# Kernel optimization log

Measured on AMD Instinct MI355X. Metric: run time of the kernel, lower is better.

## Reference

```python
import jax, jax.numpy as jnp
import numpy as np
from math import sqrt

B, S, D, H = 2, 2048, 1024, 16
HD = D // H


def setup_inputs() -> dict:
    key = jax.random.key(0)
    ks = jax.random.split(key, 5)
    std = 0.02
    return {
        "tensor_in": jax.random.normal(ks[0], (B, S, D), dtype=jnp.float32),
        "attention_mask": jnp.zeros((1, 1, S, S), dtype=jnp.float32),
        "Wq": jax.random.normal(ks[1], (D, D), dtype=jnp.float32) * std,
        "Wk": jax.random.normal(ks[2], (D, D), dtype=jnp.float32) * std,
        "Wv": jax.random.normal(ks[3], (D, D), dtype=jnp.float32) * std,
        "Wo": jax.random.normal(ks[4], (D, D), dtype=jnp.float32) * std,
    }


def reference(tensor_in, attention_mask, Wq, Wk, Wv, Wo):
    # nn.Linear(dim, dim, bias=False): y = x @ W.T, W is [out, in]
    q = tensor_in @ Wq.T  # [B,S,D]
    k = tensor_in @ Wk.T
    v = tensor_in @ Wv.T
    # split heads -> [B,H,S,HD]
    q = q.reshape(B, S, H, HD).transpose(0, 2, 1, 3)
    k = k.reshape(B, S, H, HD).transpose(0, 2, 1, 3)
    v = v.reshape(B, S, H, HD).transpose(0, 2, 1, 3)
    # scores [B,H,S,S]; note: mask added BEFORE scaling, scale = sqrt(full dim)
    scores = jnp.einsum("bhqd,bhkd->bhqk", q, k) + attention_mask
    weights = jax.nn.softmax(scores / sqrt(D), axis=-1)  # dropout = identity (eval)
    context = jnp.einsum("bhqk,bhkd->bhqd", weights, v)
    context = context.transpose(0, 2, 1, 3).reshape(B, S, D)
    return context @ Wo.T
```

## Files before the change

kernel.cpp:

```cpp
#include <hip/hip_runtime.h>

#define B_  2
#define S_  2048
#define D_  1024
#define H_  16
#define HD_ 64
#define M_  (B_*S_)

typedef __attribute__((ext_vector_type(8))) short  short8;
typedef __attribute__((ext_vector_type(4))) float  float4v;
typedef __attribute__((ext_vector_type(4))) int    int4v;
typedef __attribute__((ext_vector_type(4))) unsigned short ushort4v;

#define PSCALE 0.0450843341f

__device__ __forceinline__ unsigned short f_to_bf16bits(float f) {
    unsigned int x = __builtin_bit_cast(unsigned int, f);
    unsigned int lsb = (x >> 16) & 1u;
    x += 0x7fffu + lsb;
    return (unsigned short)(x >> 16);
}

__device__ __forceinline__ float fast_exp2(float x) {
#if __has_builtin(__builtin_amdgcn_exp2f)
    return __builtin_amdgcn_exp2f(x);
#else
    return exp2f(x);
#endif
}

__global__ __launch_bounds__(256) void cvt_bf16(
    const float* __restrict__ X,  const float* __restrict__ Wq,
    const float* __restrict__ Wk, const float* __restrict__ Wv,
    const float* __restrict__ Wo,
    unsigned short* __restrict__ Xb,  unsigned short* __restrict__ Wqb,
    unsigned short* __restrict__ Wkb, unsigned short* __restrict__ Wvb,
    unsigned short* __restrict__ Wob)
{
    const long t = (long)blockIdx.x * 256 + threadIdx.x;
    const long e = t * 8;
    const float* src; unsigned short* dst; long off;
    if      (e < 4194304) { src = X;  dst = Xb;  off = e; }
    else if (e < 5242880) { src = Wq; dst = Wqb; off = e - 4194304; }
    else if (e < 6291456) { src = Wk; dst = Wkb; off = e - 5242880; }
    else if (e < 7340032) { src = Wv; dst = Wvb; off = e - 6291456; }
    else                  { src = Wo; dst = Wob; off = e - 7340032; }
    float4v a = *(const float4v*)&src[off];
    float4v b = *(const float4v*)&src[off + 4];
    int4v o;
    o[0] = (int)f_to_bf16bits(a[0]) | ((int)f_to_bf16bits(a[1]) << 16);
    o[1] = (int)f_to_bf16bits(a[2]) | ((int)f_to_bf16bits(a[3]) << 16);
    o[2] = (int)f_to_bf16bits(b[0]) | ((int)f_to_bf16bits(b[1]) << 16);
    o[3] = (int)f_to_bf16bits(b[2]) | ((int)f_to_bf16bits(b[3]) << 16);
    *(int4v*)&dst[off] = o;
}

__global__ __launch_bounds__(256) void gemm_bt(
    const unsigned short* __restrict__ A,
    const unsigned short* __restrict__ B0,
    const unsigned short* __restrict__ B1,
    const unsigned short* __restrict__ B2,
    void* __restrict__ O0, void* __restrict__ O1, void* __restrict__ O2,
    int mode_base)
{
    const int K = 1024;
    const int z = blockIdx.z;
    const int mode = mode_base + z;
    const unsigned short* Aop;
    const unsigned short* Bop;
    void* Op = (z == 0) ? O0 : (z == 1) ? O1 : O2;
    int m0, n0;
    if (mode == 2) {
        Aop = B2; Bop = A;
        m0 = blockIdx.y * 128;
        n0 = blockIdx.x * 128;
    } else {
        Aop = A;
        Bop = (z == 0) ? B0 : (z == 1) ? B1 : B2;
        m0 = blockIdx.x * 128;
        n0 = blockIdx.y * 128;
    }

    __shared__ alignas(16) unsigned short As[128 * 64];
    __shared__ alignas(16) unsigned short Bs[128 * 64];

    const int tid  = threadIdx.x;
    const int wv   = tid >> 6;
    const int lane = tid & 63;
    const int wm   = wv >> 1, wn = wv & 1;
    const int q4   = lane >> 4, l15 = lane & 15;

    const unsigned short* gA[4];
    const unsigned short* gB[4];
    int ldsoff[4];
#pragma unroll
    for (int j = 0; j < 4; j++) {
        const int r = wv * 32 + j * 8 + (lane >> 3);
        const int c = (((lane & 7) ^ (r & 7)) * 8);
        gA[j] = Aop + (long)(m0 + r) * K + c;
        gB[j] = Bop + (long)(n0 + r) * K + c;
        ldsoff[j] = (wv * 32 + j * 8) * 64 + lane * 8;
    }

    int aoff[2][4], boff[2][4];
#pragma unroll
    for (int ks = 0; ks < 2; ks++)
#pragma unroll
        for (int t = 0; t < 4; t++) {
            const int swz = (((ks * 4 + q4) ^ (l15 & 7)) * 8);
            aoff[ks][t] = (wm * 64 + t * 16 + l15) * 64 + swz;
            boff[ks][t] = (wn * 64 + t * 16 + l15) * 64 + swz;
        }

    float4v acc[4][4];
#pragma unroll
    for (int i = 0; i < 4; i++)
#pragma unroll
        for (int j = 0; j < 4; j++) acc[i][j] = (float4v)0.0f;

    int4v ar[4], br[4];
#pragma unroll
    for (int j = 0; j < 4; j++) {
        ar[j] = *(const int4v*)gA[j];
        br[j] = *(const int4v*)gB[j];
        gA[j] += 64; gB[j] += 64;
    }

    for (int k0 = 0; k0 < K; k0 += 64) {
        __syncthreads();
#pragma unroll
        for (int j = 0; j < 4; j++) {
            *(int4v*)&As[ldsoff[j]] = ar[j];
            *(int4v*)&Bs[ldsoff[j]] = br[j];
        }
        __syncthreads();

        if (k0 + 64 < K) {
#pragma unroll
            for (int j = 0; j < 4; j++) {
                ar[j] = *(const int4v*)gA[j];
                br[j] = *(const int4v*)gB[j];
                gA[j] += 64; gB[j] += 64;
            }
        }

#pragma unroll
        for (int ks = 0; ks < 2; ks++) {
            short8 afr[4], bfr[4];
#pragma unroll
            for (int mt = 0; mt < 4; mt++) afr[mt] = *(const short8*)&As[aoff[ks][mt]];
#pragma unroll
            for (int nt = 0; nt < 4; nt++) bfr[nt] = *(const short8*)&Bs[boff[ks][nt]];
#pragma unroll
            for (int mt = 0; mt < 4; mt++)
#pragma unroll
                for (int nt = 0; nt < 4; nt++)
                    acc[mt][nt] = __builtin_amdgcn_mfma_f32_16x16x32_bf16(
                        afr[mt], bfr[nt], acc[mt][nt], 0, 0, 0);
        }
    }

#pragma unroll
    for (int mt = 0; mt < 4; mt++)
#pragma unroll
        for (int nt = 0; nt < 4; nt++)
#pragma unroll
            for (int r = 0; r < 4; r++) {
                const int m = m0 + wm * 64 + mt * 16 + q4 * 4 + r;
                const int n = n0 + wn * 64 + nt * 16 + l15;
                float v = acc[mt][nt][r];
                if (mode == 3) {
                    ((float*)Op)[(long)m * D_ + n] = v;
                } else if (mode == 2) {
                    const long off = (((long)(n >> 11) * H_ + (m >> 6)) * HD_ + (m & 63)) * S_ + (n & 2047);
                    ((unsigned short*)Op)[off] = f_to_bf16bits(v);
                } else {
                    const long off = ((long)((m >> 11) * H_ + (n >> 6)) * S_ + (m & 2047)) * HD_ + (n & 63);
                    if (mode == 0) v *= PSCALE;
                    ((unsigned short*)Op)[off] = f_to_bf16bits(v);
                }
            }
}

__global__ __launch_bounds__(256) void attn(
    const unsigned short* __restrict__ Q,
    const unsigned short* __restrict__ Kk,
    const unsigned short* __restrict__ Vt,
    const float* __restrict__ mask,
    unsigned short* __restrict__ ctx)
{
    __shared__ alignas(16) unsigned short Ks[64 * 64];
    __shared__ alignas(16) unsigned short Vs[64 * 64];
    __shared__ alignas(16) unsigned short Ps[4][16 * 64];

    const int tid  = threadIdx.x;
    const int wv   = tid >> 6;
    const int lane = tid & 63;
    const int q4   = lane >> 4, l15 = lane & 15;
    const int bh   = blockIdx.x;
    const int q0   = blockIdx.y * 64;

    const long head = (long)bh * S_ * HD_;

    const int qrow = q0 + wv * 16 + l15;
    short8 qfr[2];
    qfr[0] = *(const short8*)&Q[head + (long)qrow * HD_ + q4 * 8];
    qfr[1] = *(const short8*)&Q[head + (long)qrow * HD_ + 32 + q4 * 8];

    float l_acc[4];
#pragma unroll
    for (int r = 0; r < 4; r++) l_acc[r] = 0.0f;
    float4v oacc[4];
#pragma unroll
    for (int dt = 0; dt < 4; dt++) oacc[dt] = (float4v)0.0f;

    const int row0 = tid >> 3, row1 = row0 + 32, sch = tid & 7;
    const int cc   = ((sch ^ (row0 & 7)) * 8);
    const unsigned short* gK0 = Kk + head + (long)row0 * HD_ + cc;
    const unsigned short* gK1 = Kk + head + (long)row1 * HD_ + cc;
    const unsigned short* gV0 = Vt + head + (long)row0 * S_  + cc;
    const unsigned short* gV1 = Vt + head + (long)row1 * S_  + cc;
    const int ldsOff0 = row0 * 64 + sch * 8;
    const int ldsOff1 = row1 * 64 + sch * 8;

    const float* mrow[4];
#pragma unroll
    for (int r = 0; r < 4; r++)
        mrow[r] = mask + (long)(q0 + wv * 16 + q4 * 4 + r) * S_ + l15;

    float mv[4][4];
#pragma unroll
    for (int nt = 0; nt < 4; nt++)
#pragma unroll
        for (int r = 0; r < 4; r++) mv[nt][r] = mrow[r][nt * 16];

    const int pswz = (q4 & 1) * 4;
    const int psl3 = l15 >> 3;

    for (int k0 = 0; k0 < S_; k0 += 64) {
        __syncthreads();
        *(int4v*)&Ks[ldsOff0] = *(const int4v*)(gK0 + (long)k0 * HD_);
        *(int4v*)&Ks[ldsOff1] = *(const int4v*)(gK1 + (long)k0 * HD_);
        *(int4v*)&Vs[ldsOff0] = *(const int4v*)(gV0 + k0);
        *(int4v*)&Vs[ldsOff1] = *(const int4v*)(gV1 + k0);
        __syncthreads();

        float4v sfr[4];
#pragma unroll
        for (int nt = 0; nt < 4; nt++) {
            const int row = nt * 16 + l15;
            const int p0 = ((q4       ^ (row & 7)) * 8);
            const int p1 = (((4 + q4) ^ (row & 7)) * 8);
            short8 kb0 = *(const short8*)&Ks[row * 64 + p0];
            short8 kb1 = *(const short8*)&Ks[row * 64 + p1];
            float4v s = (float4v)0.0f;
            s = __builtin_amdgcn_mfma_f32_16x16x32_bf16(qfr[0], kb0, s, 0, 0, 0);
            s = __builtin_amdgcn_mfma_f32_16x16x32_bf16(qfr[1], kb1, s, 0, 0, 0);
            sfr[nt] = s;
        }

        float mvn[4][4];
        const int knext = (k0 + 64 < S_) ? k0 + 64 : k0;
#pragma unroll
        for (int nt = 0; nt < 4; nt++)
#pragma unroll
            for (int r = 0; r < 4; r++) mvn[nt][r] = mrow[r][knext + nt * 16];

#pragma unroll
        for (int nt = 0; nt < 4; nt++)
#pragma unroll
            for (int r = 0; r < 4; r++) {
                const float p = fast_exp2(fmaf(mv[nt][r], PSCALE, sfr[nt][r]));
                l_acc[r] += p;
                const int c8 = (nt * 2 + psl3) ^ (pswz + r);
                Ps[wv][(q4 * 4 + r) * 64 + c8 * 8 + (l15 & 7)] = f_to_bf16bits(p);
            }

        const int pp0 = ((q4       ^ (l15 & 7)) * 8);
        const int pp1 = (((4 + q4) ^ (l15 & 7)) * 8);
        short8 pf0 = *(const short8*)&Ps[wv][l15 * 64 + pp0];
        short8 pf1 = *(const short8*)&Ps[wv][l15 * 64 + pp1];

#pragma unroll
        for (int dt = 0; dt < 4; dt++) {
            const int row = dt * 16 + l15;
            const int p0 = ((q4       ^ (row & 7)) * 8);
            const int p1 = (((4 + q4) ^ (row & 7)) * 8);
            short8 vb0 = *(const short8*)&Vs[row * 64 + p0];
            short8 vb1 = *(const short8*)&Vs[row * 64 + p1];
            float4v o = oacc[dt];
            o = __builtin_amdgcn_mfma_f32_16x16x32_bf16(pf0, vb0, o, 0, 0, 0);
            o = __builtin_amdgcn_mfma_f32_16x16x32_bf16(pf1, vb1, o, 0, 0, 0);
            oacc[dt] = o;
        }

#pragma unroll
        for (int nt = 0; nt < 4; nt++)
#pragma unroll
            for (int r = 0; r < 4; r++) mv[nt][r] = mvn[nt][r];
    }

#pragma unroll
    for (int r = 0; r < 4; r++) {
#pragma unroll
        for (int off = 1; off < 16; off <<= 1)
            l_acc[r] += __shfl_xor(l_acc[r], off);
    }

    const int b = bh >> 4, h = bh & 15;
#pragma unroll
    for (int dt = 0; dt < 4; dt++)
#pragma unroll
        for (int r = 0; r < 4; r++) {
            const int qg = q0 + wv * 16 + q4 * 4 + r;
            const int d  = dt * 16 + l15;
            const float v = oacc[dt][r] / l_acc[r];
            ctx[((long)(b * S_ + qg)) * D_ + h * HD_ + d] = f_to_bf16bits(v);
        }
}

extern "C" void kernel_launch(void* const* d_in, const int* in_sizes, int n_in,
                              void* d_out, int out_size, void* d_ws, size_t ws_size,
                              hipStream_t stream) {
    const float* X    = (const float*)d_in[0];
    const float* mask = (const float*)d_in[1];
    const float* Wq   = (const float*)d_in[2];
    const float* Wk   = (const float*)d_in[3];
    const float* Wv   = (const float*)d_in[4];
    const float* Wo   = (const float*)d_in[5];
    float* out        = (float*)d_out;

    unsigned short* ws = (unsigned short*)d_ws;
    unsigned short* qws  = ws;
    unsigned short* kws  = ws + 4194304;
    unsigned short* vtws = ws + 8388608;
    unsigned short* ctx  = ws + 12582912;
    unsigned short* Xb   = ws + 16777216;
    unsigned short* Wqb  = ws + 20971520;
    unsigned short* Wkb  = ws + 22020096;
    unsigned short* Wvb  = ws + 23068672;
    unsigned short* Wob  = ws + 24117248;

    cvt_bf16<<<dim3(4096), 256, 0, stream>>>(X, Wq, Wk, Wv, Wo, Xb, Wqb, Wkb, Wvb, Wob);
    gemm_bt<<<dim3(32, 8, 3), 256, 0, stream>>>(Xb, Wqb, Wkb, Wvb, qws, kws, vtws, 0);
    attn<<<dim3(32, 32, 1), 256, 0, stream>>>(qws, kws, vtws, mask, ctx);
    gemm_bt<<<dim3(32, 8, 1), 256, 0, stream>>>(ctx, Wob, Wob, Wob, out, out, out, 3);
}
```

Baseline: 235.9 us.

## Double attention KV tile to 128 keys and use packed bf16 conversion

```diff
diff --git a/kernel.cpp b/kernel.cpp
--- a/kernel.cpp
+++ b/kernel.cpp
@@ -14,11 +14,26 @@
 
 #define PSCALE 0.0450843341f
 
+__device__ __forceinline__ unsigned int pack2_bf16(float a, float b) {
+#if __has_builtin(__builtin_amdgcn_cvt_pk_bf16_f32)
+    auto p = __builtin_amdgcn_cvt_pk_bf16_f32(a, b);
+    return __builtin_bit_cast(unsigned int, p);
+#else
+    unsigned int xa = __builtin_bit_cast(unsigned int, a);
+    unsigned int xb = __builtin_bit_cast(unsigned int, b);
+    xa += 0x7fffu + ((xa >> 16) & 1u);
+    xb += 0x7fffu + ((xb >> 16) & 1u);
+    return (xa >> 16) | (xb & 0xffff0000u);
+#endif
+}
 __device__ __forceinline__ unsigned short f_to_bf16bits(float f) {
+#if __has_builtin(__builtin_amdgcn_cvt_pk_bf16_f32)
+    return (unsigned short)(pack2_bf16(f, f) & 0xffffu);
+#else
     unsigned int x = __builtin_bit_cast(unsigned int, f);
-    unsigned int lsb = (x >> 16) & 1u;
-    x += 0x7fffu + lsb;
+    x += 0x7fffu + ((x >> 16) & 1u);
     return (unsigned short)(x >> 16);
+#endif
 }
 
 __device__ __forceinline__ float fast_exp2(float x) {
@@ -48,10 +63,10 @@
     float4v a = *(const float4v*)&src[off];
     float4v b = *(const float4v*)&src[off + 4];
     int4v o;
-    o[0] = (int)f_to_bf16bits(a[0]) | ((int)f_to_bf16bits(a[1]) << 16);
-    o[1] = (int)f_to_bf16bits(a[2]) | ((int)f_to_bf16bits(a[3]) << 16);
-    o[2] = (int)f_to_bf16bits(b[0]) | ((int)f_to_bf16bits(b[1]) << 16);
-    o[3] = (int)f_to_bf16bits(b[2]) | ((int)f_to_bf16bits(b[3]) << 16);
+    o[0] = (int)pack2_bf16(a[0], a[1]);
+    o[1] = (int)pack2_bf16(a[2], a[3]);
+    o[2] = (int)pack2_bf16(b[0], b[1]);
+    o[3] = (int)pack2_bf16(b[2], b[3]);
     *(int4v*)&dst[off] = o;
 }
 
@@ -189,8 +204,8 @@
     const float* __restrict__ mask,
     unsigned short* __restrict__ ctx)
 {
-    __shared__ alignas(16) unsigned short Ks[64 * 64];
-    __shared__ alignas(16) unsigned short Vs[64 * 64];
+    __shared__ alignas(16) unsigned short Ks[128 * 64];
+    __shared__ alignas(16) unsigned short Vs[64 * 128];
     __shared__ alignas(16) unsigned short Ps[4][16 * 64];
 
     const int tid  = threadIdx.x;
@@ -214,14 +229,24 @@
 #pragma unroll
     for (int dt = 0; dt < 4; dt++) oacc[dt] = (float4v)0.0f;
 
-    const int row0 = tid >> 3, row1 = row0 + 32, sch = tid & 7;
-    const int cc   = ((sch ^ (row0 & 7)) * 8);
-    const unsigned short* gK0 = Kk + head + (long)row0 * HD_ + cc;
-    const unsigned short* gK1 = Kk + head + (long)row1 * HD_ + cc;
-    const unsigned short* gV0 = Vt + head + (long)row0 * S_  + cc;
-    const unsigned short* gV1 = Vt + head + (long)row1 * S_  + cc;
-    const int ldsOff0 = row0 * 64 + sch * 8;
-    const int ldsOff1 = row1 * 64 + sch * 8;
+    const int krow = tid >> 3, ksch = tid & 7;
+    const unsigned short* gK[4];
+    int kldso[4];
+#pragma unroll
+    for (int j = 0; j < 4; j++) {
+        const int row = j * 32 + krow;
+        gK[j] = Kk + head + (long)row * HD_ + ((ksch ^ (row & 7)) * 8);
+        kldso[j] = row * 64 + ksch * 8;
+    }
+    const int vrow = tid >> 4, vl = tid & 15;
+    const unsigned short* gV[4];
+    int vldso[4];
+#pragma unroll
+    for (int j = 0; j < 4; j++) {
+        const int row = j * 16 + vrow;
+        gV[j] = Vt + head + (long)row * S_ + vl * 8;
+        vldso[j] = row * 128 + (((vl & 8) | ((vl & 7) ^ (row & 7))) * 8);
+    }
 
     const float* mrow[4];
 #pragma unroll
@@ -236,68 +261,71 @@
 
     const int pswz = (q4 & 1) * 4;
     const int psl3 = l15 >> 3;
-
-    for (int k0 = 0; k0 < S_; k0 += 64) {
+    const int kp0 = ((q4       ^ (l15 & 7)) * 8);
+    const int kp1 = (((4 + q4) ^ (l15 & 7)) * 8);
+
+    for (int k0 = 0; k0 < S_; k0 += 128) {
         __syncthreads();
-        *(int4v*)&Ks[ldsOff0] = *(const int4v*)(gK0 + (long)k0 * HD_);
-        *(int4v*)&Ks[ldsOff1] = *(const int4v*)(gK1 + (long)k0 * HD_);
-        *(int4v*)&Vs[ldsOff0] = *(const int4v*)(gV0 + k0);
-        *(int4v*)&Vs[ldsOff1] = *(const int4v*)(gV1 + k0);
+#pragma unroll
+        for (int j = 0; j < 4; j++)
+            *(int4v*)&Ks[kldso[j]] = *(const int4v*)(gK[j] + (long)k0 * HD_);
+#pragma unroll
+        for (int j = 0; j < 4; j++)
+            *(int4v*)&Vs[vldso[j]] = *(const int4v*)(gV[j] + k0);
         __syncthreads();
 
-        float4v sfr[4];
-#pragma unroll
-        for (int nt = 0; nt < 4; nt++) {
-            const int row = nt * 16 + l15;
-            const int p0 = ((q4       ^ (row & 7)) * 8);
-            const int p1 = (((4 + q4) ^ (row & 7)) * 8);
-            short8 kb0 = *(const short8*)&Ks[row * 64 + p0];
-            short8 kb1 = *(const short8*)&Ks[row * 64 + p1];
-            float4v s = (float4v)0.0f;
-            s = __builtin_amdgcn_mfma_f32_16x16x32_bf16(qfr[0], kb0, s, 0, 0, 0);
-            s = __builtin_amdgcn_mfma_f32_16x16x32_bf16(qfr[1], kb1, s, 0, 0, 0);
-            sfr[nt] = s;
-        }
-
-        float mvn[4][4];
-        const int knext = (k0 + 64 < S_) ? k0 + 64 : k0;
-#pragma unroll
-        for (int nt = 0; nt < 4; nt++)
-#pragma unroll
-            for (int r = 0; r < 4; r++) mvn[nt][r] = mrow[r][knext + nt * 16];
-
-#pragma unroll
-        for (int nt = 0; nt < 4; nt++)
-#pragma unroll
-            for (int r = 0; r < 4; r++) {
-                const float p = fast_exp2(fmaf(mv[nt][r], PSCALE, sfr[nt][r]));
-                l_acc[r] += p;
-                const int c8 = (nt * 2 + psl3) ^ (pswz + r);
-                Ps[wv][(q4 * 4 + r) * 64 + c8 * 8 + (l15 & 7)] = f_to_bf16bits(p);
+#pragma unroll
+        for (int h = 0; h < 2; h++) {
+            const int kb = k0 + h * 64;
+
+            float4v sfr[4];
+#pragma unroll
+            for (int nt = 0; nt < 4; nt++) {
+                const int row = h * 64 + nt * 16 + l15;
+                short8 kb0 = *(const short8*)&Ks[row * 64 + kp0];
+                short8 kb1 = *(const short8*)&Ks[row * 64 + kp1];
+                float4v s = (float4v)0.0f;
+                s = __builtin_amdgcn_mfma_f32_16x16x32_bf16(qfr[0], kb0, s, 0, 0, 0);
+                s = __builtin_amdgcn_mfma_f32_16x16x32_bf16(qfr[1], kb1, s, 0, 0, 0);
+                sfr[nt] = s;
             }
 
-        const int pp0 = ((q4       ^ (l15 & 7)) * 8);
-        const int pp1 = (((4 + q4) ^ (l15 & 7)) * 8);
-        short8 pf0 = *(const short8*)&Ps[wv][l15 * 64 + pp0];
-        short8 pf1 = *(const short8*)&Ps[wv][l15 * 64 + pp1];
-
-#pragma unroll
-        for (int dt = 0; dt < 4; dt++) {
-            const int row = dt * 16 + l15;
-            const int p0 = ((q4       ^ (row & 7)) * 8);
-            const int p1 = (((4 + q4) ^ (row & 7)) * 8);
-            short8 vb0 = *(const short8*)&Vs[row * 64 + p0];
-            short8 vb1 = *(const short8*)&Vs[row * 64 + p1];
-            float4v o = oacc[dt];
-            o = __builtin_amdgcn_mfma_f32_16x16x32_bf16(pf0, vb0, o, 0, 0, 0);
-            o = __builtin_amdgcn_mfma_f32_16x16x32_bf16(pf1, vb1, o, 0, 0, 0);
-            oacc[dt] = o;
-        }
-
-#pragma unroll
-        for (int nt = 0; nt < 4; nt++)
-#pragma unroll
-            for (int r = 0; r < 4; r++) mv[nt][r] = mvn[nt][r];
+            float mvn[4][4];
+            const int knext = (kb + 64 < S_) ? kb + 64 : kb;
+#pragma unroll
+            for (int nt = 0; nt < 4; nt++)
+#pragma unroll
+                for (int r = 0; r < 4; r++) mvn[nt][r] = mrow[r][knext + nt * 16];
+
+#pragma unroll
+            for (int nt = 0; nt < 4; nt++)
+#pragma unroll
+                for (int r = 0; r < 4; r++) {
+                    const float p = fast_exp2(fmaf(mv[nt][r], PSCALE, sfr[nt][r]));
+                    l_acc[r] += p;
+                    const int c8 = (nt * 2 + psl3) ^ (pswz + r);
+                    Ps[wv][(q4 * 4 + r) * 64 + c8 * 8 + (l15 & 7)] = f_to_bf16bits(p);
+                }
+
+            short8 pf0 = *(const short8*)&Ps[wv][l15 * 64 + kp0];
+            short8 pf1 = *(const short8*)&Ps[wv][l15 * 64 + kp1];
+
+#pragma unroll
+            for (int dt = 0; dt < 4; dt++) {
+                const int row = dt * 16 + l15;
+                short8 vb0 = *(const short8*)&Vs[row * 128 + h * 64 + kp0];
+                short8 vb1 = *(const short8*)&Vs[row * 128 + h * 64 + kp1];
+                float4v o = oacc[dt];
+                o = __builtin_amdgcn_mfma_f32_16x16x32_bf16(pf0, vb0, o, 0, 0, 0);
+                o = __builtin_amdgcn_mfma_f32_16x16x32_bf16(pf1, vb1, o, 0, 0, 0);
+                oacc[dt] = o;
+            }
+
+#pragma unroll
+            for (int nt = 0; nt < 4; nt++)
+#pragma unroll
+                for (int r = 0; r < 4; r++) mv[nt][r] = mvn[nt][r];
+        }
     }
 
 #pragma unroll
```

After: 273.9 us. +16.1%, slower.
